# Optimization experiments

Hardware: AMD Instinct MI355X
Metric: run time of the kernel (lower is better)

Reference implementation:

```python
import jax, jax.numpy as jnp
import numpy as np

N_NODES = 50000
N_EDGES = 800000
IN_DIM = 128
HID = 64
N_LAYERS = 4  # num_layers=5 in source -> 4 GINConv layers
BN_EPS = 1e-5


def setup_inputs() -> dict:
    key = jax.random.key(0)
    ks = jax.random.split(key, 16)
    h = jax.random.normal(ks[0], (N_NODES, IN_DIM), dtype=jnp.float32)
    src = jax.random.randint(ks[1], (N_EDGES,), 0, N_NODES, dtype=jnp.int32)
    dst = jax.random.randint(ks[2], (N_EDGES,), 0, N_NODES, dtype=jnp.int32)
    s = 0.05
    # layer 0 params (IN_DIM -> HID -> HID)
    W1_0 = jax.random.normal(ks[3], (IN_DIM, HID), dtype=jnp.float32) * s
    b1_0 = jnp.zeros((HID,), jnp.float32)
    W2_0 = jax.random.normal(ks[4], (HID, HID), dtype=jnp.float32) * s
    b2_0 = jnp.zeros((HID,), jnp.float32)
    g_0 = jnp.ones((HID,), jnp.float32)
    be_0 = jnp.zeros((HID,), jnp.float32)
    # layers 1..3 params stacked (HID -> HID -> HID)
    W1s = jax.random.normal(ks[5], (N_LAYERS - 1, HID, HID), dtype=jnp.float32) * s
    b1s = jnp.zeros((N_LAYERS - 1, HID), jnp.float32)
    W2s = jax.random.normal(ks[6], (N_LAYERS - 1, HID, HID), dtype=jnp.float32) * s
    b2s = jnp.zeros((N_LAYERS - 1, HID), jnp.float32)
    gs = jnp.ones((N_LAYERS - 1, HID), jnp.float32)
    bes = jnp.zeros((N_LAYERS - 1, HID), jnp.float32)
    return dict(h=h, src=src, dst=dst,
                W1_0=W1_0, b1_0=b1_0, W2_0=W2_0, b2_0=b2_0, g_0=g_0, be_0=be_0,
                W1s=W1s, b1s=b1s, W2s=W2s, b2s=b2s, gs=gs, bes=bes)


def _gin_layer(h, src, dst, W1, b1, W2, b2, gamma, beta):
    # GINConv (eps=0, sum aggregation): z = h + sum_{j->i} h_j
    agg = jax.ops.segment_sum(h[src], dst, num_segments=N_NODES)  # [N, d]
    z = h + agg
    # MLP: Linear -> ReLU -> Linear
    z = jax.nn.relu(z @ W1 + b1) @ W2 + b2
    # BatchNorm1d (training mode: batch statistics over nodes)
    mean = jnp.mean(z, axis=0)
    var = jnp.var(z, axis=0)
    z = (z - mean) * jax.lax.rsqrt(var + BN_EPS) * gamma + beta
    return jax.nn.relu(z)


def reference(h, src, dst, W1_0, b1_0, W2_0, b2_0, g_0, be_0,
              W1s, b1s, W2s, b2s, gs, bes):
    h = _gin_layer(h, src, dst, W1_0, b1_0, W2_0, b2_0, g_0, be_0)
    for i in range(N_LAYERS - 1):
        h = _gin_layer(h, src, dst, W1s[i], b1s[i], W2s[i], b2s[i], gs[i], bes[i])
    return h
```

## Files before the change

kernel.cpp:

```cpp
#include <hip/hip_runtime.h>
#include <hip/hip_bf16.h>

static constexpr int NN = 50000;
static constexpr int NE = 800000;
static constexpr float BN_EPS = 1e-5f;

static constexpr int NB  = 128;
static constexpr int NPB = 391;
static constexpr int CAP = 8192;
static constexpr int CHUNK = 2048;

__device__ __forceinline__ float bflo(unsigned u) { return __uint_as_float(u << 16); }
__device__ __forceinline__ float bfhi(unsigned u) { return __uint_as_float(u & 0xffff0000u); }
__device__ __forceinline__ unsigned short f2bf(float f) {
    unsigned u = __float_as_uint(f);
    unsigned r = (u + 0x7fffu + ((u >> 16) & 1u)) >> 16;
    return (unsigned short)r;
}

__global__ __launch_bounds__(256) void zero_kernel(int* __restrict__ ptr, int n)
{
    int i = blockIdx.x * 256 + threadIdx.x;
    if (i < n) ptr[i] = 0;
}

__global__ __launch_bounds__(256) void binA_kernel(
    const int* __restrict__ src, const int* __restrict__ dst,
    int* __restrict__ gcount, unsigned long long* __restrict__ tmp)
{
    __shared__ unsigned long long stage[CHUNK];
    __shared__ int hist[NB], base[NB], gpos[NB];

    const int t = threadIdx.x;
    const int cb = blockIdx.x * CHUNK;
    const int total = min(CHUNK, NE - cb);

    if (t < NB) hist[t] = 0;
    __syncthreads();

    int mb[8], mslot[8];
    unsigned long long mv[8];
    #pragma unroll
    for (int k = 0; k < 8; ++k) {
        int e = cb + k * 256 + t;
        mb[k] = -1;
        if (e < NE) {
            int s = src[e];
            int d = dst[e];
            int b = d / NPB;
            mb[k] = b;
            mv[k] = ((unsigned long long)(unsigned)d << 32) | (unsigned)s;
            mslot[k] = atomicAdd(&hist[b], 1);
        }
    }
    __syncthreads();

    if (t < NB) base[t] = hist[t];
    __syncthreads();
    for (int ofs = 1; ofs < NB; ofs <<= 1) {
        int v = (t >= ofs && t < NB) ? base[t - ofs] : 0;
        __syncthreads();
        if (t < NB) base[t] += v;
        __syncthreads();
    }
    if (t < NB && hist[t] > 0)
        gpos[t] = t * CAP + atomicAdd(&gcount[t], hist[t]);
    __syncthreads();

    #pragma unroll
    for (int k = 0; k < 8; ++k) {
        if (mb[k] >= 0) {
            int b = mb[k];
            stage[(base[b] - hist[b]) + mslot[k]] = mv[k];
        }
    }
    __syncthreads();

    for (int i = t; i < total; i += 256) {
        unsigned long long v = stage[i];
        int b = (int)(v >> 32) / NPB;
        int pos = gpos[b] + (i - (base[b] - hist[b]));
        tmp[pos] = v;
    }
}

__global__ __launch_bounds__(256) void binB_kernel(
    const unsigned long long* __restrict__ tmp, const int* __restrict__ gcount,
    int* __restrict__ off, int* __restrict__ eidx)
{
    __shared__ int gb[NB];
    __shared__ int hist[NPB];
    __shared__ int hs[512];
    __shared__ int cur[NPB];
    __shared__ int base_s;

    const int t = threadIdx.x;
    const int b = blockIdx.x;
    const int n0 = b * NPB;
    const int n1 = min(n0 + NPB, NN);
    const int nnodes = n1 - n0;
    const int cnt = gcount[b];

    if (t < NB) gb[t] = gcount[t];
    for (int n = t; n < NPB; n += 256) hist[n] = 0;
    __syncthreads();
    for (int ofs = 1; ofs < NB; ofs <<= 1) {
        int v = (t >= ofs && t < NB) ? gb[t - ofs] : 0;
        __syncthreads();
        if (t < NB) gb[t] += v;
        __syncthreads();
    }
    if (t == 0) base_s = (b == 0) ? 0 : gb[b - 1];
    __syncthreads();
    const int base = base_s;

    const unsigned long long* tb = tmp + (size_t)b * CAP;
    for (int i = t; i < cnt; i += 256) {
        int d = (int)(tb[i] >> 32);
        atomicAdd(&hist[d - n0], 1);
    }
    __syncthreads();
    hs[t] = (t < NPB) ? hist[t] : 0;
    hs[t + 256] = (t + 256 < NPB) ? hist[t + 256] : 0;
    __syncthreads();
    for (int ofs = 1; ofs < 512; ofs <<= 1) {
        int a0 = (t >= ofs) ? hs[t - ofs] : 0;
        int a1 = hs[t + 256 - ofs];
        __syncthreads();
        hs[t] += a0;
        hs[t + 256] += a1;
        __syncthreads();
    }
    for (int n = t; n < nnodes; n += 256) {
        int excl = hs[n] - hist[n];
        off[n0 + n] = base + excl;
        cur[n] = base + excl;
    }
    if (b == NB - 1 && t == 0) off[NN] = base + cnt;
    __syncthreads();
    for (int i = t; i < cnt; i += 256) {
        unsigned long long v = tb[i];
        int d = (int)(v >> 32);
        int pos = atomicAdd(&cur[d - n0], 1);
        eidx[pos] = (int)(v & 0xffffffffu);
    }
}

template<int D, bool NORM>
__global__ __launch_bounds__(256) void proj_kernel(
    const float* __restrict__ hin, const float* __restrict__ W1,
    const float* __restrict__ gsum, const float* __restrict__ gsq,
    const float* __restrict__ gamma, const float* __restrict__ beta,
    unsigned short* __restrict__ p)
{
    constexpr int RPB = 128;
    __shared__ float XsT[64][132];
    __shared__ float Ws[64][64];
    __shared__ float scs[64], shs[64];

    const int t = threadIdx.x;
    const int rowbase = blockIdx.x * RPB;

    if (NORM) {
        if (t < 64) {
            const float invn = 1.f / (float)NN;
            float mean = gsum[t] * invn;
            float var  = gsq[t] * invn - mean * mean;
            float sc   = gamma[t] * rsqrtf(var + BN_EPS);
            scs[t] = sc;
            shs[t] = beta[t] - mean * sc;
        }
        __syncthreads();
    }

    const int tc = t & 7;
    const int tr = t >> 3;
    const int c0 = tc * 8;
    const int r0 = tr * 4;

    float acc[4][8];
    #pragma unroll
    for (int i = 0; i < 4; ++i)
        #pragma unroll
        for (int j = 0; j < 8; ++j) acc[i][j] = 0.f;

    for (int kc = 0; kc < D; kc += 64) {
        if (kc) __syncthreads();
        {
            const float4* wg = reinterpret_cast<const float4*>(W1 + (size_t)kc * 64);
            float4* wl = reinterpret_cast<float4*>(&Ws[0][0]);
            for (int i = t; i < 64 * 16; i += 256) wl[i] = wg[i];
        }
        {
            int rr = t & 15, q = t >> 4;
            for (int i = 0; i < RPB; i += 16) {
                int r = i + rr;
                int gr = rowbase + r;
                float4 v = make_float4(0.f, 0.f, 0.f, 0.f);
                if (gr < NN) {
                    v = reinterpret_cast<const float4*>(hin + (size_t)gr * D + kc)[q];
                    if (NORM) {
                        int c = q * 4;
                        v.x = fmaxf(v.x * scs[c + 0] + shs[c + 0], 0.f);
                        v.y = fmaxf(v.y * scs[c + 1] + shs[c + 1], 0.f);
                        v.z = fmaxf(v.z * scs[c + 2] + shs[c + 2], 0.f);
                        v.w = fmaxf(v.w * scs[c + 3] + shs[c + 3], 0.f);
                    }
                }
                XsT[q * 4 + 0][r] = v.x;
                XsT[q * 4 + 1][r] = v.y;
                XsT[q * 4 + 2][r] = v.z;
                XsT[q * 4 + 3][r] = v.w;
            }
        }
        __syncthreads();

        for (int k = 0; k < 64; ++k) {
            float4 xa = *reinterpret_cast<const float4*>(&XsT[k][r0]);
            float4 wa = *reinterpret_cast<const float4*>(&Ws[k][c0]);
            float4 wb = *reinterpret_cast<const float4*>(&Ws[k][c0 + 4]);
            float x[4] = { xa.x, xa.y, xa.z, xa.w };
            float w[8] = { wa.x, wa.y, wa.z, wa.w, wb.x, wb.y, wb.z, wb.w };
            #pragma unroll
            for (int i = 0; i < 4; ++i)
                #pragma unroll
                for (int j = 0; j < 8; ++j) acc[i][j] += x[i] * w[j];
        }
    }

    #pragma unroll
    for (int i = 0; i < 4; ++i) {
        int gr = rowbase + r0 + i;
        if (gr < NN) {
            uint4 u;
            u.x = (unsigned)f2bf(acc[i][0]) | ((unsigned)f2bf(acc[i][1]) << 16);
            u.y = (unsigned)f2bf(acc[i][2]) | ((unsigned)f2bf(acc[i][3]) << 16);
            u.z = (unsigned)f2bf(acc[i][4]) | ((unsigned)f2bf(acc[i][5]) << 16);
            u.w = (unsigned)f2bf(acc[i][6]) | ((unsigned)f2bf(acc[i][7]) << 16);
            *reinterpret_cast<uint4*>(p + (size_t)gr * 64 + c0) = u;
        }
    }
}

__global__ __launch_bounds__(256) void gather_kernel(
    const unsigned short* __restrict__ p, const int* __restrict__ off,
    const int* __restrict__ eidx, const float* __restrict__ b1,
    unsigned short* __restrict__ Y)
{
    int gid = blockIdx.x * 256 + threadIdx.x;
    if (gid >= NN * 8) return;
    int row = gid >> 3;
    int q = gid & 7;

    const uint4* pb = reinterpret_cast<const uint4*>(p);
    uint4 u = pb[row * 8 + q];
    float a0 = bflo(u.x), a1 = bfhi(u.x), a2 = bflo(u.y), a3 = bfhi(u.y);
    float a4 = bflo(u.z), a5 = bfhi(u.z), a6 = bflo(u.w), a7 = bfhi(u.w);

    int e = off[row];
    const int end = off[row + 1];
    for (; e + 4 <= end; e += 4) {
        int s0 = eidx[e + 0], s1 = eidx[e + 1];
        int s2 = eidx[e + 2], s3 = eidx[e + 3];
        uint4 v0 = pb[s0 * 8 + q];
        uint4 v1 = pb[s1 * 8 + q];
        uint4 v2 = pb[s2 * 8 + q];
        uint4 v3 = pb[s3 * 8 + q];
        a0 += (bflo(v0.x) + bflo(v1.x)) + (bflo(v2.x) + bflo(v3.x));
        a1 += (bfhi(v0.x) + bfhi(v1.x)) + (bfhi(v2.x) + bfhi(v3.x));
        a2 += (bflo(v0.y) + bflo(v1.y)) + (bflo(v2.y) + bflo(v3.y));
        a3 += (bfhi(v0.y) + bfhi(v1.y)) + (bfhi(v2.y) + bfhi(v3.y));
        a4 += (bflo(v0.z) + bflo(v1.z)) + (bflo(v2.z) + bflo(v3.z));
        a5 += (bfhi(v0.z) + bfhi(v1.z)) + (bfhi(v2.z) + bfhi(v3.z));
        a6 += (bflo(v0.w) + bflo(v1.w)) + (bflo(v2.w) + bflo(v3.w));
        a7 += (bfhi(v0.w) + bfhi(v1.w)) + (bfhi(v2.w) + bfhi(v3.w));
    }
    for (; e < end; ++e) {
        uint4 v = pb[eidx[e] * 8 + q];
        a0 += bflo(v.x); a1 += bfhi(v.x); a2 += bflo(v.y); a3 += bfhi(v.y);
        a4 += bflo(v.z); a5 += bfhi(v.z); a6 += bflo(v.w); a7 += bfhi(v.w);
    }

    float4 blo = reinterpret_cast<const float4*>(b1)[q * 2];
    float4 bhi = reinterpret_cast<const float4*>(b1)[q * 2 + 1];
    a0 = fmaxf(a0 + blo.x, 0.f); a1 = fmaxf(a1 + blo.y, 0.f);
    a2 = fmaxf(a2 + blo.z, 0.f); a3 = fmaxf(a3 + blo.w, 0.f);
    a4 = fmaxf(a4 + bhi.x, 0.f); a5 = fmaxf(a5 + bhi.y, 0.f);
    a6 = fmaxf(a6 + bhi.z, 0.f); a7 = fmaxf(a7 + bhi.w, 0.f);

    uint4 o;
    o.x = (unsigned)f2bf(a0) | ((unsigned)f2bf(a1) << 16);
    o.y = (unsigned)f2bf(a2) | ((unsigned)f2bf(a3) << 16);
    o.z = (unsigned)f2bf(a4) | ((unsigned)f2bf(a5) << 16);
    o.w = (unsigned)f2bf(a6) | ((unsigned)f2bf(a7) << 16);
    reinterpret_cast<uint4*>(Y)[row * 8 + q] = o;
}

__global__ __launch_bounds__(256) void mlp2_kernel(
    const unsigned short* __restrict__ Y, const float* __restrict__ W2,
    const float* __restrict__ b2, float* __restrict__ z,
    float* __restrict__ gsum, float* __restrict__ gsq)
{
    constexpr int RPB = 128;
    __shared__ float XsT[64][132];
    __shared__ float Ws[64][64];
    __shared__ float b2s[64], lsum[64], lsq[64];

    const int t = threadIdx.x;
    const int rowbase = blockIdx.x * RPB;

    if (t < 64) { b2s[t] = b2[t]; lsum[t] = 0.f; lsq[t] = 0.f; }

    {
        const float4* wg = reinterpret_cast<const float4*>(W2);
        float4* wl = reinterpret_cast<float4*>(&Ws[0][0]);
        for (int i = t; i < 64 * 16; i += 256) wl[i] = wg[i];
    }
    {
        const uint4* yb = reinterpret_cast<const uint4*>(Y);
        int rr = t & 31, qq = t >> 5;
        for (int i = 0; i < RPB; i += 32) {
            int r = i + rr;
            int gr = rowbase + r;
            uint4 v = make_uint4(0u, 0u, 0u, 0u);
            if (gr < NN) v = yb[gr * 8 + qq];
            int c = qq * 8;
            XsT[c + 0][r] = bflo(v.x); XsT[c + 1][r] = bfhi(v.x);
            XsT[c + 2][r] = bflo(v.y); XsT[c + 3][r] = bfhi(v.y);
            XsT[c + 4][r] = bflo(v.z); XsT[c + 5][r] = bfhi(v.z);
            XsT[c + 6][r] = bflo(v.w); XsT[c + 7][r] = bfhi(v.w);
        }
    }
    __syncthreads();

    const int tc = t & 7;
    const int tr = t >> 3;
    const int c0 = tc * 8;
    const int r0 = tr * 4;

    float acc[4][8];
    #pragma unroll
    for (int i = 0; i < 4; ++i)
        #pragma unroll
        for (int j = 0; j < 8; ++j) acc[i][j] = 0.f;

    for (int k = 0; k < 64; ++k) {
        float4 xa = *reinterpret_cast<const float4*>(&XsT[k][r0]);
        float4 wa = *reinterpret_cast<const float4*>(&Ws[k][c0]);
        float4 wb = *reinterpret_cast<const float4*>(&Ws[k][c0 + 4]);
        float x[4] = { xa.x, xa.y, xa.z, xa.w };
        float w[8] = { wa.x, wa.y, wa.z, wa.w, wb.x, wb.y, wb.z, wb.w };
        #pragma unroll
        for (int i = 0; i < 4; ++i)
            #pragma unroll
            for (int j = 0; j < 8; ++j) acc[i][j] += x[i] * w[j];
    }

    float s[8], sq[8];
    #pragma unroll
    for (int j = 0; j < 8; ++j) { s[j] = 0.f; sq[j] = 0.f; }

    #pragma unroll
    for (int i = 0; i < 4; ++i) {
        int gr = rowbase + r0 + i;
        if (gr < NN) {
            float zv[8];
            #pragma unroll
            for (int j = 0; j < 8; ++j) {
                zv[j] = acc[i][j] + b2s[c0 + j];
                s[j] += zv[j];
                sq[j] += zv[j] * zv[j];
            }
            float4 lo = make_float4(zv[0], zv[1], zv[2], zv[3]);
            float4 hi = make_float4(zv[4], zv[5], zv[6], zv[7]);
            *reinterpret_cast<float4*>(z + (size_t)gr * 64 + c0) = lo;
            *reinterpret_cast<float4*>(z + (size_t)gr * 64 + c0 + 4) = hi;
        }
    }

    #pragma unroll
    for (int j = 0; j < 8; ++j) {
        s[j]  += __shfl_xor(s[j], 8);
        s[j]  += __shfl_xor(s[j], 16);
        s[j]  += __shfl_xor(s[j], 32);
        sq[j] += __shfl_xor(sq[j], 8);
        sq[j] += __shfl_xor(sq[j], 16);
        sq[j] += __shfl_xor(sq[j], 32);
    }
    if ((t & 56) == 0) {
        #pragma unroll
        for (int j = 0; j < 8; ++j) {
            atomicAdd(&lsum[c0 + j], s[j]);
            atomicAdd(&lsq[c0 + j], sq[j]);
        }
    }
    __syncthreads();
    if (t < 64) {
        atomicAdd(&gsum[t], lsum[t]);
        atomicAdd(&gsq[t], lsq[t]);
    }
}

__global__ __launch_bounds__(256) void norm_kernel(
    const float* __restrict__ z,
    const float* __restrict__ gsum, const float* __restrict__ gsq,
    const float* __restrict__ gamma, const float* __restrict__ beta,
    float* __restrict__ out)
{
    __shared__ float sc[64], sh[64];
    int t = threadIdx.x;
    if (t < 64) {
        const float invn = 1.f / (float)NN;
        float mean = gsum[t] * invn;
        float var  = gsq[t] * invn - mean * mean;
        float s    = gamma[t] * rsqrtf(var + BN_EPS);
        sc[t] = s;
        sh[t] = beta[t] - mean * s;
    }
    __syncthreads();
    int idx = blockIdx.x * 256 + t;
    if (idx >= NN * 16) return;
    int c = (idx & 15) * 4;
    float4 v = reinterpret_cast<const float4*>(z)[idx];
    v.x = fmaxf(v.x * sc[c + 0] + sh[c + 0], 0.f);
    v.y = fmaxf(v.y * sc[c + 1] + sh[c + 1], 0.f);
    v.z = fmaxf(v.z * sc[c + 2] + sh[c + 2], 0.f);
    v.w = fmaxf(v.w * sc[c + 3] + sh[c + 3], 0.f);
    reinterpret_cast<float4*>(out)[idx] = v;
}

extern "C" void kernel_launch(void* const* d_in, const int* in_sizes, int n_in,
                              void* d_out, int out_size, void* d_ws, size_t ws_size,
                              hipStream_t stream)
{
    const float* h    = (const float*)d_in[0];
    const int*   src  = (const int*)d_in[1];
    const int*   dst  = (const int*)d_in[2];
    const float* W1_0 = (const float*)d_in[3];
    const float* b1_0 = (const float*)d_in[4];
    const float* W2_0 = (const float*)d_in[5];
    const float* b2_0 = (const float*)d_in[6];
    const float* g_0  = (const float*)d_in[7];
    const float* be_0 = (const float*)d_in[8];
    const float* W1st = (const float*)d_in[9];
    const float* b1st = (const float*)d_in[10];
    const float* W2st = (const float*)d_in[11];
    const float* b2st = (const float*)d_in[12];
    const float* gst  = (const float*)d_in[13];
    const float* best = (const float*)d_in[14];
    float* out = (float*)d_out;

    char* ws = (char*)d_ws;
    unsigned short* p = (unsigned short*)ws;
    unsigned short* Y = p + (size_t)NN * 64;
    unsigned long long* tmp = (unsigned long long*)(Y + (size_t)NN * 64);
    int* eidx   = (int*)(tmp + (size_t)NB * CAP);
    float* stats = (float*)(eidx + NE);
    int* gcount = (int*)(stats + 512);
    int* off    = gcount + NB;
    float* z    = out;

    zero_kernel<<<3, 256, 0, stream>>>((int*)stats, 512 + NB);
    binA_kernel<<<(NE + CHUNK - 1) / CHUNK, 256, 0, stream>>>(src, dst, gcount, tmp);
    binB_kernel<<<NB, 256, 0, stream>>>(tmp, gcount, off, eidx);

    const int gemmblk   = (NN + 127) / 128;
    const int gatherblk = (NN * 8 + 255) / 256;
    const int thrblk    = (NN * 16 + 255) / 256;

    float* gs0 = stats + 0 * 128;
    proj_kernel<128, false><<<gemmblk, 256, 0, stream>>>(
        h, W1_0, nullptr, nullptr, nullptr, nullptr, p);
    gather_kernel<<<gatherblk, 256, 0, stream>>>(p, off, eidx, b1_0, Y);
    mlp2_kernel<<<gemmblk, 256, 0, stream>>>(Y, W2_0, b2_0, z, gs0, gs0 + 64);

    const float* gammas[4] = { g_0, gst + 0, gst + 64, gst + 128 };
    const float* betas[4]  = { be_0, best + 0, best + 64, best + 128 };

    for (int l = 0; l < 3; ++l) {
        float* gsp = stats + l * 128;
        float* gsc = stats + (l + 1) * 128;
        proj_kernel<64, true><<<gemmblk, 256, 0, stream>>>(
            z, W1st + l * 4096, gsp, gsp + 64, gammas[l], betas[l], p);
        gather_kernel<<<gatherblk, 256, 0, stream>>>(p, off, eidx, b1st + l * 64, Y);
        mlp2_kernel<<<gemmblk, 256, 0, stream>>>(
            Y, W2st + l * 4096, b2st + l * 64, z, gsc, gsc + 64);
    }

    float* gs3 = stats + 3 * 128;
    norm_kernel<<<thrblk, 256, 0, stream>>>(z, gs3, gs3 + 64, gammas[3], betas[3], out);
}
```

Measured before the change: 258.0 us.

## Store intermediate activations in bf16 and pack edge keys into 32 bits

The per-layer MLP output z is now written as bf16 into a workspace buffer instead of fp32 into the output. The next layer's projection and the final norm kernel read and unpack it, with BN statistics still accumulated in fp32 before rounding. Edge binning packs (dst, src) into one 32-bit word instead of 64 bits, which relies on node ids fitting in 16 bits. Both changes cut memory traffic, at the cost of bf16 rounding error on the stored activations and a hard node-count limit of 65536.

```diff
diff --git a/kernel.cpp b/kernel.cpp
--- a/kernel.cpp
+++ b/kernel.cpp
@@ -26,9 +26,9 @@
 
 __global__ __launch_bounds__(256) void binA_kernel(
     const int* __restrict__ src, const int* __restrict__ dst,
-    int* __restrict__ gcount, unsigned long long* __restrict__ tmp)
-{
-    __shared__ unsigned long long stage[CHUNK];
+    int* __restrict__ gcount, unsigned* __restrict__ tmp)
+{
+    __shared__ unsigned stage[CHUNK];
     __shared__ int hist[NB], base[NB], gpos[NB];
 
     const int t = threadIdx.x;
@@ -39,7 +39,7 @@
     __syncthreads();
 
     int mb[8], mslot[8];
-    unsigned long long mv[8];
+    unsigned mv[8];
     #pragma unroll
     for (int k = 0; k < 8; ++k) {
         int e = cb + k * 256 + t;
@@ -49,7 +49,7 @@
             int d = dst[e];
             int b = d / NPB;
             mb[k] = b;
-            mv[k] = ((unsigned long long)(unsigned)d << 32) | (unsigned)s;
+            mv[k] = ((unsigned)d << 16) | (unsigned)s;
             mslot[k] = atomicAdd(&hist[b], 1);
         }
     }
@@ -77,15 +77,15 @@
     __syncthreads();
 
     for (int i = t; i < total; i += 256) {
-        unsigned long long v = stage[i];
-        int b = (int)(v >> 32) / NPB;
+        unsigned v = stage[i];
+        int b = (int)(v >> 16) / NPB;
         int pos = gpos[b] + (i - (base[b] - hist[b]));
         tmp[pos] = v;
     }
 }
 
 __global__ __launch_bounds__(256) void binB_kernel(
-    const unsigned long long* __restrict__ tmp, const int* __restrict__ gcount,
+    const unsigned* __restrict__ tmp, const int* __restrict__ gcount,
     int* __restrict__ off, int* __restrict__ eidx)
 {
     __shared__ int gb[NB];
@@ -114,9 +114,9 @@
     __syncthreads();
     const int base = base_s;
 
-    const unsigned long long* tb = tmp + (size_t)b * CAP;
+    const unsigned* tb = tmp + (size_t)b * CAP;
     for (int i = t; i < cnt; i += 256) {
-        int d = (int)(tb[i] >> 32);
+        int d = (int)(tb[i] >> 16);
         atomicAdd(&hist[d - n0], 1);
     }
     __syncthreads();
@@ -139,16 +139,16 @@
     if (b == NB - 1 && t == 0) off[NN] = base + cnt;
     __syncthreads();
     for (int i = t; i < cnt; i += 256) {
-        unsigned long long v = tb[i];
-        int d = (int)(v >> 32);
+        unsigned v = tb[i];
+        int d = (int)(v >> 16);
         int pos = atomicAdd(&cur[d - n0], 1);
-        eidx[pos] = (int)(v & 0xffffffffu);
+        eidx[pos] = (int)(v & 0xffffu);
     }
 }
 
 template<int D, bool NORM>
 __global__ __launch_bounds__(256) void proj_kernel(
-    const float* __restrict__ hin, const float* __restrict__ W1,
+    const void* __restrict__ hin_, const float* __restrict__ W1,
     const float* __restrict__ gsum, const float* __restrict__ gsq,
     const float* __restrict__ gamma, const float* __restrict__ beta,
     unsigned short* __restrict__ p)
@@ -191,22 +191,35 @@
             float4* wl = reinterpret_cast<float4*>(&Ws[0][0]);
             for (int i = t; i < 64 * 16; i += 256) wl[i] = wg[i];
         }
-        {
+        if constexpr (NORM) {
+            const uint4* hb = reinterpret_cast<const uint4*>(hin_);
+            int rr = t & 31, q = t >> 5;
+            for (int i = 0; i < RPB; i += 32) {
+                int r = i + rr;
+                int gr = rowbase + r;
+                uint4 v = make_uint4(0u, 0u, 0u, 0u);
+                if (gr < NN) v = hb[gr * 8 + q];
+                int c = q * 8;
+                float f0 = bflo(v.x), f1 = bfhi(v.x), f2 = bflo(v.y), f3 = bfhi(v.y);
+                float f4 = bflo(v.z), f5 = bfhi(v.z), f6 = bflo(v.w), f7 = bfhi(v.w);
+                XsT[c + 0][r] = fmaxf(f0 * scs[c + 0] + shs[c + 0], 0.f);
+                XsT[c + 1][r] = fmaxf(f1 * scs[c + 1] + shs[c + 1], 0.f);
+                XsT[c + 2][r] = fmaxf(f2 * scs[c + 2] + shs[c + 2], 0.f);
+                XsT[c + 3][r] = fmaxf(f3 * scs[c + 3] + shs[c + 3], 0.f);
+                XsT[c + 4][r] = fmaxf(f4 * scs[c + 4] + shs[c + 4], 0.f);
+                XsT[c + 5][r] = fmaxf(f5 * scs[c + 5] + shs[c + 5], 0.f);
+                XsT[c + 6][r] = fmaxf(f6 * scs[c + 6] + shs[c + 6], 0.f);
+                XsT[c + 7][r] = fmaxf(f7 * scs[c + 7] + shs[c + 7], 0.f);
+            }
+        } else {
+            const float* hin = reinterpret_cast<const float*>(hin_);
             int rr = t & 15, q = t >> 4;
             for (int i = 0; i < RPB; i += 16) {
                 int r = i + rr;
                 int gr = rowbase + r;
                 float4 v = make_float4(0.f, 0.f, 0.f, 0.f);
-                if (gr < NN) {
+                if (gr < NN)
                     v = reinterpret_cast<const float4*>(hin + (size_t)gr * D + kc)[q];
-                    if (NORM) {
-                        int c = q * 4;
-                        v.x = fmaxf(v.x * scs[c + 0] + shs[c + 0], 0.f);
-                        v.y = fmaxf(v.y * scs[c + 1] + shs[c + 1], 0.f);
-                        v.z = fmaxf(v.z * scs[c + 2] + shs[c + 2], 0.f);
-                        v.w = fmaxf(v.w * scs[c + 3] + shs[c + 3], 0.f);
-                    }
-                }
                 XsT[q * 4 + 0][r] = v.x;
                 XsT[q * 4 + 1][r] = v.y;
                 XsT[q * 4 + 2][r] = v.z;
@@ -298,7 +311,7 @@
 
 __global__ __launch_bounds__(256) void mlp2_kernel(
     const unsigned short* __restrict__ Y, const float* __restrict__ W2,
-    const float* __restrict__ b2, float* __restrict__ z,
+    const float* __restrict__ b2, unsigned short* __restrict__ zb,
     float* __restrict__ gsum, float* __restrict__ gsq)
 {
     constexpr int RPB = 128;
@@ -371,10 +384,12 @@
                 s[j] += zv[j];
                 sq[j] += zv[j] * zv[j];
             }
-            float4 lo = make_float4(zv[0], zv[1], zv[2], zv[3]);
-            float4 hi = make_float4(zv[4], zv[5], zv[6], zv[7]);
-            *reinterpret_cast<float4*>(z + (size_t)gr * 64 + c0) = lo;
-            *reinterpret_cast<float4*>(z + (size_t)gr * 64 + c0 + 4) = hi;
+            uint4 o;
+            o.x = (unsigned)f2bf(zv[0]) | ((unsigned)f2bf(zv[1]) << 16);
+            o.y = (unsigned)f2bf(zv[2]) | ((unsigned)f2bf(zv[3]) << 16);
+            o.z = (unsigned)f2bf(zv[4]) | ((unsigned)f2bf(zv[5]) << 16);
+            o.w = (unsigned)f2bf(zv[6]) | ((unsigned)f2bf(zv[7]) << 16);
+            *reinterpret_cast<uint4*>(zb + (size_t)gr * 64 + c0) = o;
         }
     }
 
@@ -402,7 +417,7 @@
 }
 
 __global__ __launch_bounds__(256) void norm_kernel(
-    const float* __restrict__ z,
+    const unsigned short* __restrict__ zb,
     const float* __restrict__ gsum, const float* __restrict__ gsq,
     const float* __restrict__ gamma, const float* __restrict__ beta,
     float* __restrict__ out)
@@ -419,14 +434,25 @@
     }
     __syncthreads();
     int idx = blockIdx.x * 256 + t;
-    if (idx >= NN * 16) return;
-    int c = (idx & 15) * 4;
-    float4 v = reinterpret_cast<const float4*>(z)[idx];
-    v.x = fmaxf(v.x * sc[c + 0] + sh[c + 0], 0.f);
-    v.y = fmaxf(v.y * sc[c + 1] + sh[c + 1], 0.f);
-    v.z = fmaxf(v.z * sc[c + 2] + sh[c + 2], 0.f);
-    v.w = fmaxf(v.w * sc[c + 3] + sh[c + 3], 0.f);
-    reinterpret_cast<float4*>(out)[idx] = v;
+    if (idx >= NN * 8) return;
+    int row = idx >> 3;
+    int q = idx & 7;
+    int c = q * 8;
+    uint4 v = reinterpret_cast<const uint4*>(zb)[idx];
+    float f0 = bflo(v.x), f1 = bfhi(v.x), f2 = bflo(v.y), f3 = bfhi(v.y);
+    float f4 = bflo(v.z), f5 = bfhi(v.z), f6 = bflo(v.w), f7 = bfhi(v.w);
+    float4 lo, hi;
+    lo.x = fmaxf(f0 * sc[c + 0] + sh[c + 0], 0.f);
+    lo.y = fmaxf(f1 * sc[c + 1] + sh[c + 1], 0.f);
+    lo.z = fmaxf(f2 * sc[c + 2] + sh[c + 2], 0.f);
+    lo.w = fmaxf(f3 * sc[c + 3] + sh[c + 3], 0.f);
+    hi.x = fmaxf(f4 * sc[c + 4] + sh[c + 4], 0.f);
+    hi.y = fmaxf(f5 * sc[c + 5] + sh[c + 5], 0.f);
+    hi.z = fmaxf(f6 * sc[c + 6] + sh[c + 6], 0.f);
+    hi.w = fmaxf(f7 * sc[c + 7] + sh[c + 7], 0.f);
+    float* o = out + (size_t)row * 64 + c;
+    *reinterpret_cast<float4*>(o) = lo;
+    *reinterpret_cast<float4*>(o + 4) = hi;
 }
 
 extern "C" void kernel_launch(void* const* d_in, const int* in_sizes, int n_in,
@@ -451,14 +477,14 @@
     float* out = (float*)d_out;
 
     char* ws = (char*)d_ws;
-    unsigned short* p = (unsigned short*)ws;
-    unsigned short* Y = p + (size_t)NN * 64;
-    unsigned long long* tmp = (unsigned long long*)(Y + (size_t)NN * 64);
+    unsigned short* p  = (unsigned short*)ws;
+    unsigned short* Y  = p + (size_t)NN * 64;
+    unsigned short* zb = Y + (size_t)NN * 64;
+    unsigned* tmp = (unsigned*)(zb + (size_t)NN * 64);
     int* eidx   = (int*)(tmp + (size_t)NB * CAP);
     float* stats = (float*)(eidx + NE);
     int* gcount = (int*)(stats + 512);
     int* off    = gcount + NB;
-    float* z    = out;
 
     zero_kernel<<<3, 256, 0, stream>>>((int*)stats, 512 + NB);
     binA_kernel<<<(NE + CHUNK - 1) / CHUNK, 256, 0, stream>>>(src, dst, gcount, tmp);
@@ -466,13 +492,13 @@
 
     const int gemmblk   = (NN + 127) / 128;
     const int gatherblk = (NN * 8 + 255) / 256;
-    const int thrblk    = (NN * 16 + 255) / 256;
+    const int normblk   = (NN * 8 + 255) / 256;
 
     float* gs0 = stats + 0 * 128;
     proj_kernel<128, false><<<gemmblk, 256, 0, stream>>>(
         h, W1_0, nullptr, nullptr, nullptr, nullptr, p);
     gather_kernel<<<gatherblk, 256, 0, stream>>>(p, off, eidx, b1_0, Y);
-    mlp2_kernel<<<gemmblk, 256, 0, stream>>>(Y, W2_0, b2_0, z, gs0, gs0 + 64);
+    mlp2_kernel<<<gemmblk, 256, 0, stream>>>(Y, W2_0, b2_0, zb, gs0, gs0 + 64);
 
     const float* gammas[4] = { g_0, gst + 0, gst + 64, gst + 128 };
     const float* betas[4]  = { be_0, best + 0, best + 64, best + 128 };
@@ -481,12 +507,12 @@
         float* gsp = stats + l * 128;
         float* gsc = stats + (l + 1) * 128;
         proj_kernel<64, true><<<gemmblk, 256, 0, stream>>>(
-            z, W1st + l * 4096, gsp, gsp + 64, gammas[l], betas[l], p);
+            zb, W1st + l * 4096, gsp, gsp + 64, gammas[l], betas[l], p);
         gather_kernel<<<gatherblk, 256, 0, stream>>>(p, off, eidx, b1st + l * 64, Y);
         mlp2_kernel<<<gemmblk, 256, 0, stream>>>(
-            Y, W2st + l * 4096, b2st + l * 64, z, gsc, gsc + 64);
+            Y, W2st + l * 4096, b2st + l * 64, zb, gsc, gsc + 64);
     }
 
     float* gs3 = stats + 3 * 128;
-    norm_kernel<<<thrblk, 256, 0, stream>>>(z, gs3, gs3 + 64, gammas[3], betas[3], out);
-}
+    norm_kernel<<<normblk, 256, 0, stream>>>(zb, gs3, gs3 + 64, gammas[3], betas[3], out);
+}
```

Result: no change. 256.2 us (-0.7%).
